# Optimization experiments

Measured on AMD Instinct MI355X. Metric: run time of the kernel, lower is better.

The kernel has to match this reference:

```python
import jax, jax.numpy as jnp
from jax import lax
import numpy as np

B, T, H, L = 4096, 7, 512, 256
D = 2 * H  # bidirectional LSTM feature dim


def _lstm(x, wih, whh, bih, bhh, reverse):
    # x: [B, T, L]; torch gate order i, f, g, o
    b, hdim = x.shape[0], whh.shape[0]
    xs = jnp.swapaxes(x, 0, 1)  # [T, B, L]
    bias = bih + bhh

    def step(carry, xt):
        h, c = carry
        gates = xt @ wih + h @ whh + bias
        i, f, g, o = jnp.split(gates, 4, axis=-1)
        c = jax.nn.sigmoid(f) * c + jax.nn.sigmoid(i) * jnp.tanh(g)
        h = jax.nn.sigmoid(o) * jnp.tanh(c)
        return (h, c), h

    h0 = jnp.zeros((b, hdim), x.dtype)
    _, hs = lax.scan(step, (h0, h0), xs, reverse=reverse)
    return jnp.swapaxes(hs, 0, 1)  # [B, T, H]


def _att(enc, dec):
    # Sequential attention: keys/values start as enc and grow with each decoder output.
    keys = enc  # [B, T, D]
    outs = []
    for i in range(dec.shape[1]):  # fixed small T=7, Python loop is static
        q = dec[:, i, :]                                  # [B, D]
        scores = jnp.einsum('bd,btd->bt', q, keys)        # dot over features
        a = jax.nn.softmax(scores, axis=1)
        ctx = jnp.einsum('bt,btd->bd', a, keys)
        out = ctx + q
        outs.append(out)
        keys = jnp.concatenate([keys, out[:, None, :]], axis=1)
    return jnp.stack(outs, axis=1)  # [B, T, D]


def _deconv(x, w, b):
    # torch ConvTranspose2d (stride 1, pad 0) == full conv with flipped, in/out-swapped kernel
    kh, kw = w.shape[2], w.shape[3]
    w2 = jnp.transpose(w[:, :, ::-1, ::-1], (1, 0, 2, 3))  # [out, in, kh, kw]
    y = lax.conv_general_dilated(x, w2, (1, 1), ((kh - 1, kh - 1), (kw - 1, kw - 1)),
                                 dimension_numbers=('NCHW', 'OIHW', 'NCHW'))
    return y + b[None, :, None, None]


def setup_inputs() -> dict:
    key = jax.random.key(0)
    ks = jax.random.split(key, 12)
    p = lambda k, shape: jax.random.normal(k, shape, jnp.float32) * 0.02
    return {
        'lstm_enc': jax.random.normal(ks[0], (B, T, D), jnp.float32),
        'gaussian_noise': jax.random.normal(ks[1], (B, L), jnp.float32),
        'embedrep_w': p(ks[2], (L, L * T)), 'embedrep_b': jnp.zeros((L * T,), jnp.float32),
        'wih_f': p(ks[3], (L, 4 * H)), 'whh_f': p(ks[4], (H, 4 * H)),
        'bih_f': jnp.zeros((4 * H,), jnp.float32), 'bhh_f': jnp.zeros((4 * H,), jnp.float32),
        'wih_b': p(ks[5], (L, 4 * H)), 'whh_b': p(ks[6], (H, 4 * H)),
        'bih_b': jnp.zeros((4 * H,), jnp.float32), 'bhh_b': jnp.zeros((4 * H,), jnp.float32),
        'emb_w': p(ks[7], (D, 1024)), 'emb_b': jnp.zeros((1024,), jnp.float32),
        'dc3_w': p(ks[8], (64, 32, 1, 3)), 'dc3_b': jnp.zeros((32,), jnp.float32),
        'dc1_w': p(ks[9], (32, 16, 1, 5)), 'dc1_b': jnp.zeros((16,), jnp.float32),
        'dc2_w': p(ks[10], (16, 1, 3, 3)), 'dc2_b': jnp.zeros((1,), jnp.float32),
        'infer': 0,
    }


def reference(lstm_enc, gaussian_noise, embedrep_w, embedrep_b,
              wih_f, whh_f, bih_f, bhh_f, wih_b, whh_b, bih_b, bhh_b,
              emb_w, emb_b, dc3_w, dc3_b, dc1_w, dc1_b, dc2_w, dc2_b, infer):
    b = lstm_enc.shape[0]
    g1 = jax.nn.soft_sign(gaussian_noise @ embedrep_w + embedrep_b)   # [B, L*T]
    rep = g1.reshape(b, T, L)                                          # [B, 7, L]
    hf = _lstm(rep, wih_f, whh_f, bih_f, bhh_f, False)
    hb = _lstm(rep, wih_b, whh_b, bih_b, bhh_b, True)
    lstm1 = jnp.concatenate([hf, hb], axis=-1)                         # [B, 7, 2H]
    att_out = _att(lstm_enc, lstm1)                                    # [B, 7, 2H]
    emb = att_out @ emb_w + emb_b                                      # [B, 7, 1024]
    up = jax.nn.soft_sign(emb).reshape(b * T, 64, 1, 16)
    x = jax.nn.leaky_relu(_deconv(up, dc3_w, dc3_b))                   # [B*7, 32, 1, 18]
    x = jax.nn.leaky_relu(_deconv(x, dc1_w, dc1_b))                    # [B*7, 16, 1, 22]
    x = jax.nn.leaky_relu(_deconv(x, dc2_w, dc2_b))                    # [B*7, 1, 3, 24]
    x = jax.nn.softmax(x, axis=2)                                      # softmax over H dim (=3)
    out = x.reshape(b, T, 1, 3, 24)[:, :, -1, :, :]                    # [B, 7, 3, 24]
    return out
```

## Files before the change

### kernel.cpp

```cpp
#include <hip/hip_runtime.h>
#include <stdint.h>


typedef __attribute__((ext_vector_type(4))) float f32x4;
typedef __attribute__((ext_vector_type(8))) short bf16x8;
typedef __attribute__((ext_vector_type(4))) unsigned short us4;

__device__ __forceinline__ unsigned short f2b(float f) {
  union { float f; unsigned u; } x; x.f = f;
  unsigned r = x.u + 0x7FFFu + ((x.u >> 16) & 1u);
  return (unsigned short)(r >> 16);
}
__device__ __forceinline__ float b2f(unsigned short s) {
  union { unsigned u; float f; } x; x.u = ((unsigned)s) << 16; return x.f;
}
__device__ __forceinline__ float sigmoidf(float x) {
  return 1.f / (1.f + __expf(-x));
}
__device__ __forceinline__ float fast_tanh(float x) {
  x = fminf(15.f, fmaxf(-15.f, x));
  float e = __expf(2.f * x);
  return (e - 1.f) / (e + 1.f);
}

__device__ __forceinline__ void gl_lds16(const void* g, void* l) {
  auto gp = reinterpret_cast<const __attribute__((address_space(1))) unsigned int*>(
      reinterpret_cast<uintptr_t>(g));
  auto lp = reinterpret_cast<__attribute__((address_space(3))) unsigned int*>(
      reinterpret_cast<uintptr_t>(l));
  __builtin_amdgcn_global_load_lds(gp, lp, 16, 0, 0);
}


__device__ __forceinline__ void stage256x32(const unsigned short* src, int ld,
                                            unsigned short* hbase, int tid) {
  const int row_in = tid >> 2;
  const int gidx = tid & 3;
#pragma unroll
  for (int r = 0; r < 4; ++r) {
    int row = r * 64 + row_in;
    int gsrc = gidx ^ ((row >> 1) & 3);
    gl_lds16(src + (size_t)row * ld + gsrc * 8, hbase + r * 2048 + (tid >> 6) * 512);
  }
}

__device__ __forceinline__ void stage128x32(const unsigned short* src, int ld,
                                            unsigned short* hbase, int tid) {
  const int row_in = tid >> 2;
  const int gidx = tid & 3;
#pragma unroll
  for (int r = 0; r < 2; ++r) {
    int row = r * 64 + row_in;
    int gsrc = gidx ^ ((row >> 1) & 3);
    gl_lds16(src + (size_t)row * ld + gsrc * 8, hbase + r * 2048 + (tid >> 6) * 512);
  }
}

__device__ __forceinline__ bf16x8 lds_fragH(const unsigned short* hbase, int row, int lq) {
  return *(const bf16x8*)(hbase + row * 32 + (lq ^ (((row >> 1) & 3) << 3)));
}

__device__ __forceinline__ void tile_w128(const unsigned short* Ab, const unsigned short* Bb,
                                          int wm, int wn, int lane, f32x4 (&acc)[8][4]) {
  const int lr = lane & 15, lq = (lane >> 4) * 8;
  bf16x8 b[4];
#pragma unroll
  for (int n = 0; n < 4; ++n) b[n] = lds_fragH(Bb, wn * 64 + n * 16 + lr, lq);
  bf16x8 a[8];
#pragma unroll
  for (int i = 0; i < 8; ++i) a[i] = lds_fragH(Ab, wm * 128 + i * 16 + lr, lq);
  __builtin_amdgcn_s_setprio(1);
#pragma unroll
  for (int i = 0; i < 8; ++i)
#pragma unroll
    for (int n = 0; n < 4; ++n)
      acc[i][n] = __builtin_amdgcn_mfma_f32_16x16x32_bf16(a[i], b[n], acc[i][n], 0, 0, 0);
  __builtin_amdgcn_s_setprio(0);
}

#define DBUF_SYNC()                                   \
  asm volatile("s_waitcnt vmcnt(0)" ::: "memory");    \
  __builtin_amdgcn_s_barrier();                       \
  __builtin_amdgcn_sched_barrier(0);

__device__ __forceinline__ void stage128x64(const unsigned short* src, int ld,
                                            unsigned short* lds, int wv, int lane) {
#pragma unroll
  for (int r = 0; r < 4; ++r) {
    int row = r * 32 + wv * 8 + (lane >> 3);
    gl_lds16(src + (size_t)row * ld + (lane & 7) * 8, lds + (r * 32 + wv * 8) * 64);
  }
}
__device__ __forceinline__ void mfma_tile(const unsigned short* As, const unsigned short* Bs,
                                          int wm, int wn, int lane, f32x4 acc[4][4]) {
#pragma unroll
  for (int kk = 0; kk < 2; ++kk) {
    int ko = kk * 32 + (lane >> 4) * 8;
    bf16x8 a[4], b[4];
#pragma unroll
    for (int i = 0; i < 4; ++i)
      a[i] = *(const bf16x8*)(As + (size_t)(wm * 64 + i * 16 + (lane & 15)) * 64 + ko);
#pragma unroll
    for (int i = 0; i < 4; ++i)
      b[i] = *(const bf16x8*)(Bs + (size_t)(wn * 64 + i * 16 + (lane & 15)) * 64 + ko);
#pragma unroll
    for (int mi = 0; mi < 4; ++mi)
#pragma unroll
      for (int ni = 0; ni < 4; ++ni)
        acc[mi][ni] = __builtin_amdgcn_mfma_f32_16x16x32_bf16(a[mi], b[ni], acc[mi][ni], 0, 0, 0);
  }
}

__global__ __launch_bounds__(256) void pack_kernel(
    const float* __restrict__ noise, const float* __restrict__ erep_w,
    const float* __restrict__ emb_w,
    const float* __restrict__ wih_f, const float* __restrict__ whh_f,
    const float* __restrict__ bih_f, const float* __restrict__ bhh_f,
    const float* __restrict__ wih_b, const float* __restrict__ whh_b,
    const float* __restrict__ bih_b, const float* __restrict__ bhh_b,
    unsigned short* __restrict__ noiseb, unsigned short* __restrict__ erepT,
    unsigned short* __restrict__ embT, unsigned short* __restrict__ lstmW,
    float* __restrict__ lstmB) {
  const int N0 = 4096 * 256 / 4;
  const int N1 = 1792 * 256 / 4;
  const int N2 = 1024 * 1024 / 4;
  const int N3 = 2 * 2048 * 768 / 4;
  const int N4 = 2 * 2048 / 4;
  const int total = N0 + N1 + N2 + N3 + N4;
  for (int i = blockIdx.x * 256 + threadIdx.x; i < total; i += gridDim.x * 256) {
    int x = i;
    if (x < N0) {
      f32x4 v = ((const f32x4*)noise)[x];
      us4 o4;
#pragma unroll
      for (int e = 0; e < 4; ++e) o4[e] = f2b(v[e]);
      ((us4*)noiseb)[x] = o4;
      continue;
    }
    x -= N0;
    if (x < N1) {
      int n = x >> 6, k4 = (x & 63) * 4;
      us4 o4;
#pragma unroll
      for (int e = 0; e < 4; ++e) o4[e] = f2b(erep_w[(size_t)(k4 + e) * 1792 + n]);
      ((us4*)erepT)[x] = o4;
      continue;
    }
    x -= N1;
    if (x < N2) {
      int n = x >> 8, k4 = (x & 255) * 4;
      int o = (n & 63) * 16 + (n >> 6);
      us4 o4;
#pragma unroll
      for (int e = 0; e < 4; ++e) o4[e] = f2b(emb_w[(size_t)(k4 + e) * 1024 + o]);
      ((us4*)embT)[x] = o4;
      continue;
    }
    x -= N2;
    if (x < N3) {
      int dir = x / (2048 * 192);
      int r = x - dir * (2048 * 192);
      int npk = r / 192, k4 = (r - npk * 192) * 4;
      int blk = npk >> 6, g = (npk >> 4) & 3, u = npk & 15;
      int o = g * 512 + blk * 16 + u;
      const float* wih = dir ? wih_b : wih_f;
      const float* whh = dir ? whh_b : whh_f;
      us4 o4;
#pragma unroll
      for (int e = 0; e < 4; ++e) {
        int k = k4 + e;
        float v = (k < 256) ? wih[(size_t)k * 2048 + o] : whh[(size_t)(k - 256) * 2048 + o];
        o4[e] = f2b(v);
      }
      ((us4*)lstmW)[x] = o4;
      continue;
    }
    x -= N3;
    {
      int dir = x >> 9, npk4 = (x & 511) * 4;
      int blk = npk4 >> 6, g = (npk4 >> 4) & 3, u = npk4 & 15;
      int o = g * 512 + blk * 16 + u;
      const float* bi = dir ? bih_b : bih_f;
      const float* bh = dir ? bhh_b : bhh_f;
      f32x4 o4;
#pragma unroll
      for (int e = 0; e < 4; ++e) o4[e] = bi[o + e] + bh[o + e];
      ((f32x4*)lstmB)[x] = o4;
    }
  }
}

__global__ __launch_bounds__(256) void gemm_rep_kernel(
    const unsigned short* __restrict__ A, const unsigned short* __restrict__ Bt,
    const float* __restrict__ bias, unsigned short* __restrict__ rep_t) {
  __shared__ unsigned short As[128 * 64];
  __shared__ unsigned short Bs[128 * 64];
  const int lane = threadIdx.x & 63, wv = threadIdx.x >> 6;
  const int wm = wv >> 1, wn = wv & 1;
  const int m0 = blockIdx.y * 128, n0 = blockIdx.x * 128;
  f32x4 acc[4][4];
#pragma unroll
  for (int i = 0; i < 4; ++i)
#pragma unroll
    for (int j = 0; j < 4; ++j) acc[i][j] = (f32x4){0.f, 0.f, 0.f, 0.f};
  for (int k0 = 0; k0 < 256; k0 += 64) {
    stage128x64(A + (size_t)m0 * 256 + k0, 256, As, wv, lane);
    stage128x64(Bt + (size_t)n0 * 256 + k0, 256, Bs, wv, lane);
    __syncthreads();
    mfma_tile(As, Bs, wm, wn, lane, acc);
    __syncthreads();
  }
#pragma unroll
  for (int ni = 0; ni < 4; ++ni) {
    int n = n0 + wn * 64 + ni * 16 + (lane & 15);
    float bv = bias[n];
    int t = n >> 8, l = n & 255;
#pragma unroll
    for (int mi = 0; mi < 4; ++mi)
#pragma unroll
      for (int r = 0; r < 4; ++r) {
        int m = m0 + wm * 64 + mi * 16 + (lane >> 4) * 4 + r;
        float v = acc[mi][ni][r] + bv;
        v = v / (1.f + fabsf(v));
        rep_t[((size_t)t * 4096 + m) * 256 + l] = f2b(v);
      }
  }
}

template <int NT>
__global__ __launch_bounds__(256, 2) void lstm_step_kernel(
    const unsigned short* __restrict__ rep_t, const unsigned short* __restrict__ Wp,
    const float* __restrict__ biasP, unsigned short* __restrict__ cbuf,
    unsigned short* __restrict__ lstm1, int step) {
  __shared__ unsigned short Ar[2][8192];
  __shared__ unsigned short Br[2][4096];
  const int tid = threadIdx.x, lane = tid & 63, wv = tid >> 6;
  const int wm = wv >> 1, wn = wv & 1;
  const int swz = (blockIdx.x & 7) * 64 + (blockIdx.x >> 3);
  const int dir = swz >> 8;
  const int rem = swz & 255;
  const int by = rem >> 4, bx = rem & 15;
  const int m0 = by * 256, n0 = bx * 128;
  const int t_proc = dir ? (6 - step) : step;
  const int t_prev = dir ? (t_proc + 1) : (t_proc - 1);
  const unsigned short* W = Wp + (size_t)dir * 2048 * 768;
  unsigned short* cp = cbuf + (size_t)dir * (4096 * 512);
  const unsigned short* xsrc = rep_t + (size_t)t_proc * 4096 * 256;
  const unsigned short* hsrc =
      lstm1 + (size_t)((NT == 24) ? t_prev : 0) * 1024 + (size_t)dir * 512;

  f32x4 acc[8][4];
#pragma unroll
  for (int i = 0; i < 8; ++i)
#pragma unroll
    for (int j = 0; j < 4; ++j) acc[i][j] = (f32x4){0.f, 0.f, 0.f, 0.f};

  auto asrc = [&](int tt) {
    return tt < 8 ? xsrc + (size_t)m0 * 256 + tt * 32
                  : hsrc + (size_t)m0 * 7168 + (tt - 8) * 32;
  };
  auto ald = [&](int tt) { return tt < 8 ? 256 : 7168; };

  stage256x32(asrc(0), ald(0), Ar[0], tid);
  stage128x32(W + (size_t)n0 * 768 + 0 * 32, 768, Br[0], tid);
  DBUF_SYNC()

#pragma unroll
  for (int t = 0; t < NT; ++t) {
    if (t + 1 < NT) {
      stage256x32(asrc(t + 1), ald(t + 1), Ar[(t + 1) & 1], tid);
      stage128x32(W + (size_t)n0 * 768 + (t + 1) * 32, 768, Br[(t + 1) & 1], tid);
    }
    tile_w128(Ar[t & 1], Br[t & 1], wm, wn, lane, acc);
    if (t + 1 < NT) { DBUF_SYNC() }
  }

  const int u = lane & 15;
  const int blk = (n0 + wn * 64) >> 6;
  const int j = blk * 16 + u;
  const float bz0 = biasP[dir * 2048 + blk * 64 + 0 * 16 + u];
  const float bz1 = biasP[dir * 2048 + blk * 64 + 1 * 16 + u];
  const float bz2 = biasP[dir * 2048 + blk * 64 + 2 * 16 + u];
  const float bz3 = biasP[dir * 2048 + blk * 64 + 3 * 16 + u];
#pragma unroll
  for (int mi = 0; mi < 8; ++mi)
#pragma unroll
    for (int r = 0; r < 4; ++r) {
      int row = m0 + wm * 128 + mi * 16 + (lane >> 4) * 4 + r;
      float gi = acc[mi][0][r] + bz0;
      float gf = acc[mi][1][r] + bz1;
      float gg = acc[mi][2][r] + bz2;
      float go = acc[mi][3][r] + bz3;
      size_t ci = (size_t)row * 512 + j;
      float c;
      if (NT == 8) {
        c = sigmoidf(gi) * fast_tanh(gg);
      } else {
        c = sigmoidf(gf) * b2f(cp[ci]) + sigmoidf(gi) * fast_tanh(gg);
      }
      cp[ci] = f2b(c);
      float h = sigmoidf(go) * fast_tanh(c);
      lstm1[((size_t)row * 7 + t_proc) * 1024 + dir * 512 + j] = f2b(h);
    }
}

__global__ __launch_bounds__(256) void att_fused3_kernel(
    const float* __restrict__ enc, const unsigned short* __restrict__ lstm1,
    unsigned short* __restrict__ att) {
  __shared__ unsigned short Qs[7 * 1032];
  __shared__ unsigned short Es[7 * 1032];
  __shared__ float P[8 * 256];
  __shared__ float sG[98];
  __shared__ float sC[7][14];
  __shared__ float sA[16];
  const int tid = threadIdx.x, lane = tid & 63, wv = tid >> 6;
  const int b = blockIdx.x;
  const float* Eb = enc + (size_t)b * 7168;
  const unsigned short* Qb = lstm1 + (size_t)b * 7168;

  if (tid < 98) ((float*)sC)[tid] = 0.f;

  const f32x4* Eb4 = (const f32x4*)Eb;
  const int d0 = tid * 4;
#pragma unroll
  for (int r = 0; r < 7; ++r) {
    f32x4 v = Eb4[r * 256 + tid];
    us4 hi;
#pragma unroll
    for (int e = 0; e < 4; ++e) hi[e] = f2b(v[e]);
    *(us4*)&Es[r * 1032 + d0] = hi;
    *(us4*)&Qs[r * 1032 + d0] = *(const us4*)(Qb + r * 1024 + d0);
  }
  asm volatile("s_waitcnt lgkmcnt(0)" ::: "memory");
  __builtin_amdgcn_sched_barrier(0);

  {
    const int rr = lane & 15;
    const int rowc = rr % 7;
    const int kbase = wv * 256 + (lane >> 4) * 8;
    f32x4 g1 = {0.f, 0.f, 0.f, 0.f}, g2 = {0.f, 0.f, 0.f, 0.f};
#pragma unroll
    for (int s = 0; s < 8; ++s) {
      const int k0 = kbase + s * 32;
      bf16x8 aq = *(const bf16x8*)&Qs[rowc * 1032 + k0];
      bf16x8 be = *(const bf16x8*)&Es[rowc * 1032 + k0];
      g1 = __builtin_amdgcn_mfma_f32_16x16x32_bf16(aq, be, g1, 0, 0, 0);
      g2 = __builtin_amdgcn_mfma_f32_16x16x32_bf16(aq, aq, g2, 0, 0, 0);
    }
    *(f32x4*)&P[((wv * 2 + 0) * 64 + lane) * 4] = g1;
    *(f32x4*)&P[((wv * 2 + 1) * 64 + lane) * 4] = g2;
  }
  __syncthreads();

  if (tid < 98) {
    int i = tid / 14, v = tid - i * 14;
    int col = v < 7 ? v : v - 7;
    int tile = v < 7 ? 0 : 1;
    int ln = ((i >> 2) << 4) | col;
    int rg = i & 3;
    float s = 0.f;
#pragma unroll
    for (int w = 0; w < 4; ++w) s += P[((w * 2 + tile) * 64 + ln) * 4 + rg];
    sG[i * 14 + v] = s;
  }
  __syncthreads();
  if (wv == 0) {
    for (int i = 0; i < 7; ++i) {
      const int nt = 7 + i;
      float s = -1e30f;
      if (lane < 7) {
        s = sG[i * 14 + lane];
      } else if (lane < nt) {
        int jj = lane - 7;
        float a2 = 0.f;
#pragma unroll
        for (int v = 0; v < 14; ++v) a2 += sC[jj][v] * sG[i * 14 + v];
        s = a2;
      }
      float mx = s;
#pragma unroll
      for (int off = 8; off >= 1; off >>= 1) mx = fmaxf(mx, __shfl_xor(mx, off, 16));
      float e = (lane < nt) ? __expf(s - mx) : 0.f;
      float sum = e;
#pragma unroll
      for (int off = 8; off >= 1; off >>= 1) sum += __shfl_xor(sum, off, 16);
      float aw = e / sum;
      if (lane < 16) sA[lane] = aw;
      if (lane < 14) {
        float c = (lane < 7) ? sA[lane] : 0.f;
        for (int jj = 0; jj < i; ++jj) c += sA[7 + jj] * sC[jj][lane];
        if (lane == 7 + i) c += 1.f;
        sC[i][lane] = c;
      }
    }
  }
  __syncthreads();

  {
    float acc[7][4];
#pragma unroll
    for (int i = 0; i < 7; ++i)
#pragma unroll
      for (int e = 0; e < 4; ++e) acc[i][e] = 0.f;
#pragma unroll
    for (int t = 0; t < 7; ++t) {
      us4 ev = *(const us4*)&Es[t * 1032 + d0];
      float evf[4];
#pragma unroll
      for (int e = 0; e < 4; ++e) evf[e] = b2f(ev[e]);
#pragma unroll
      for (int i = 0; i < 7; ++i) {
        float c = sC[i][t];
#pragma unroll
        for (int e = 0; e < 4; ++e) acc[i][e] += c * evf[e];
      }
    }
#pragma unroll
    for (int m = 0; m < 7; ++m) {
      us4 qv = *(const us4*)&Qs[m * 1032 + d0];
      float qf[4];
#pragma unroll
      for (int e = 0; e < 4; ++e) qf[e] = b2f(qv[e]);
#pragma unroll
      for (int i = m; i < 7; ++i) {
        float c = sC[i][7 + m];
#pragma unroll
        for (int e = 0; e < 4; ++e) acc[i][e] += c * qf[e];
      }
    }
    unsigned short* Ab = att + (size_t)b * 7168;
#pragma unroll
    for (int i = 0; i < 7; ++i) {
      us4 r;
#pragma unroll
      for (int e = 0; e < 4; ++e) r[e] = f2b(acc[i][e]);
      *(us4*)(Ab + i * 1024 + d0) = r;
    }
  }
}

__global__ __launch_bounds__(256, 2) void gemm_emb_kernel(
    const unsigned short* __restrict__ A, const unsigned short* __restrict__ Bt,
    const float* __restrict__ bias, unsigned short* __restrict__ up_t) {
  __shared__ unsigned short Ar[2][8192];
  __shared__ unsigned short Br[2][4096];
  const int tid = threadIdx.x, lane = tid & 63, wv = tid >> 6;
  const int wm = wv >> 1, wn = wv & 1;
  const int swz = (blockIdx.x & 7) * 112 + (blockIdx.x >> 3);
  const int by = swz >> 3, bx = swz & 7;
  const int m0 = by * 256, n0 = bx * 128;

  f32x4 acc[8][4];
#pragma unroll
  for (int i = 0; i < 8; ++i)
#pragma unroll
    for (int j = 0; j < 4; ++j) acc[i][j] = (f32x4){0.f, 0.f, 0.f, 0.f};

  const unsigned short* Abase = A + (size_t)m0 * 1024;
  const unsigned short* Bbase = Bt + (size_t)n0 * 1024;

  stage256x32(Abase + 0 * 32, 1024, Ar[0], tid);
  stage128x32(Bbase + 0 * 32, 1024, Br[0], tid);
  DBUF_SYNC()

#pragma unroll
  for (int t = 0; t < 32; ++t) {
    if (t + 1 < 32) {
      stage256x32(Abase + (t + 1) * 32, 1024, Ar[(t + 1) & 1], tid);
      stage128x32(Bbase + (t + 1) * 32, 1024, Br[(t + 1) & 1], tid);
    }
    tile_w128(Ar[t & 1], Br[t & 1], wm, wn, lane, acc);
    if (t + 1 < 32) { DBUF_SYNC() }
  }

#pragma unroll
  for (int ni = 0; ni < 4; ++ni) {
    int np = n0 + wn * 64 + ni * 16 + (lane & 15);
    int o = (np & 63) * 16 + (np >> 6);
    float bv = bias[o];
#pragma unroll
    for (int mi = 0; mi < 8; ++mi)
#pragma unroll
      for (int r = 0; r < 4; ++r) {
        int m = m0 + wm * 128 + mi * 16 + (lane >> 4) * 4 + r;
        float v = acc[mi][ni][r] + bv;
        v = v / (1.f + fabsf(v));
        up_t[(size_t)m * 1024 + np] = f2b(v);
      }
  }
}

__global__ __launch_bounds__(256) void dc_fused_kernel(
    const unsigned short* __restrict__ up_t,
    const float* __restrict__ w3, const float* __restrict__ b3,
    const float* __restrict__ w1, const float* __restrict__ b1,
    const float* __restrict__ w2, const float* __restrict__ b2,
    float* __restrict__ out) {
  __shared__ unsigned short y1L[576 * 40];
  __shared__ unsigned short y2L[704 * 24];
  const int tid = threadIdx.x, lane = tid & 63, wv = tid >> 6;
  const int g0 = blockIdx.x * 32;
  const int kq = (lane >> 4) * 8;
  const int oc = lane & 15;

  {
    bf16x8 bf[2][6];
#pragma unroll
    for (int nt = 0; nt < 2; ++nt)
#pragma unroll
      for (int kk = 0; kk < 6; ++kk) {
        bf16x8 v;
#pragma unroll
        for (int t = 0; t < 8; ++t) {
          int k = kk * 32 + kq + t;
          int jj = k >> 6, ic = k & 63;
          v[t] = (short)f2b(w3[((size_t)ic * 32 + nt * 16 + oc) * 3 + jj]);
        }
        bf[nt][kk] = v;
      }
    const float bia0 = b3[oc], bia1 = b3[16 + oc];
    for (int c = wv; c < 36; c += 4) {
      int m = c * 16 + (lane & 15);
      int imgl = m / 18, ow = m - imgl * 18;
      const unsigned short* arow = up_t + (size_t)(g0 + imgl) * 1024;
      f32x4 acc0 = {0.f, 0.f, 0.f, 0.f}, acc1 = {0.f, 0.f, 0.f, 0.f};
#pragma unroll
      for (int kk = 0; kk < 6; ++kk) {
        int jj = kk >> 1;
        int ic0 = (kk & 1) * 32 + kq;
        int iw = ow - jj;
        bf16x8 a = {0, 0, 0, 0, 0, 0, 0, 0};
        if ((unsigned)iw < 16u) a = *(const bf16x8*)(arow + iw * 64 + ic0);
        acc0 = __builtin_amdgcn_mfma_f32_16x16x32_bf16(a, bf[0][kk], acc0, 0, 0, 0);
        acc1 = __builtin_amdgcn_mfma_f32_16x16x32_bf16(a, bf[1][kk], acc1, 0, 0, 0);
      }
#pragma unroll
      for (int r = 0; r < 4; ++r) {
        int mm = c * 16 + (lane >> 4) * 4 + r;
        float v0 = acc0[r] + bia0; v0 = v0 > 0.f ? v0 : 0.01f * v0;
        float v1 = acc1[r] + bia1; v1 = v1 > 0.f ? v1 : 0.01f * v1;
        y1L[mm * 40 + oc] = f2b(v0);
        y1L[mm * 40 + 16 + oc] = f2b(v1);
      }
    }
  }
  __syncthreads();

  {
    bf16x8 bf[5];
#pragma unroll
    for (int kk = 0; kk < 5; ++kk) {
      bf16x8 v;
#pragma unroll
      for (int t = 0; t < 8; ++t) {
        int ic = kq + t;
        v[t] = (short)f2b(w1[((size_t)ic * 16 + oc) * 5 + kk]);
      }
      bf[kk] = v;
    }
    const float bia = b1[oc];
    for (int c = wv; c < 44; c += 4) {
      int m = c * 16 + (lane & 15);
      int imgl = m / 22, ow = m - imgl * 22;
      const unsigned short* abase = y1L + imgl * (18 * 40);
      f32x4 acc = {0.f, 0.f, 0.f, 0.f};
#pragma unroll
      for (int kk = 0; kk < 5; ++kk) {
        int iw = ow - kk;
        bf16x8 a = {0, 0, 0, 0, 0, 0, 0, 0};
        if ((unsigned)iw < 18u) a = *(const bf16x8*)(abase + iw * 40 + kq);
        acc = __builtin_amdgcn_mfma_f32_16x16x32_bf16(a, bf[kk], acc, 0, 0, 0);
      }
#pragma unroll
      for (int r = 0; r < 4; ++r) {
        int mm = c * 16 + (lane >> 4) * 4 + r;
        float v = acc[r] + bia;
        v = v > 0.f ? v : 0.01f * v;
        y2L[mm * 24 + oc] = f2b(v);
      }
    }
  }
  __syncthreads();

  for (int ii = tid; ii < 768; ii += 256) {
    int imgl = ii / 24, ow = ii - imgl * 24;
    float lg0 = b2[0], lg1 = b2[0], lg2 = b2[0];
#pragma unroll
    for (int jj = 0; jj < 3; ++jj) {
      int iw = ow - jj;
      if ((unsigned)iw >= 22u) continue;
      const unsigned short* row = y2L + (imgl * 22 + iw) * 24;
      bf16x8 v0 = *(const bf16x8*)(row);
      bf16x8 v1 = *(const bf16x8*)(row + 8);
      float x[16];
#pragma unroll
      for (int ic = 0; ic < 8; ++ic) {
        x[ic] = b2f((unsigned short)v0[ic]);
        x[8 + ic] = b2f((unsigned short)v1[ic]);
      }
#pragma unroll
      for (int ic = 0; ic < 16; ++ic) {
        lg0 += x[ic] * w2[ic * 9 + 0 * 3 + jj];
        lg1 += x[ic] * w2[ic * 9 + 1 * 3 + jj];
        lg2 += x[ic] * w2[ic * 9 + 2 * 3 + jj];
      }
    }
    lg0 = lg0 > 0.f ? lg0 : 0.01f * lg0;
    lg1 = lg1 > 0.f ? lg1 : 0.01f * lg1;
    lg2 = lg2 > 0.f ? lg2 : 0.01f * lg2;
    float mx = fmaxf(lg0, fmaxf(lg1, lg2));
    float e0 = __expf(lg0 - mx), e1 = __expf(lg1 - mx), e2 = __expf(lg2 - mx);
    float inv = 1.f / (e0 + e1 + e2);
    size_t ob = (size_t)(g0 + imgl) * 72 + ow;
    out[ob] = e0 * inv;
    out[ob + 24] = e1 * inv;
    out[ob + 48] = e2 * inv;
  }
}

extern "C" void kernel_launch(void* const* d_in, const int* in_sizes, int n_in,
                              void* d_out, int out_size, void* d_ws, size_t ws_size,
                              hipStream_t stream) {
  (void)in_sizes; (void)n_in; (void)out_size; (void)ws_size;
  const float* enc    = (const float*)d_in[0];
  const float* noise  = (const float*)d_in[1];
  const float* erep_w = (const float*)d_in[2];
  const float* erep_b = (const float*)d_in[3];
  const float* wih_f  = (const float*)d_in[4];
  const float* whh_f  = (const float*)d_in[5];
  const float* bih_f  = (const float*)d_in[6];
  const float* bhh_f  = (const float*)d_in[7];
  const float* wih_b  = (const float*)d_in[8];
  const float* whh_b  = (const float*)d_in[9];
  const float* bih_b  = (const float*)d_in[10];
  const float* bhh_b  = (const float*)d_in[11];
  const float* emb_w  = (const float*)d_in[12];
  const float* emb_b  = (const float*)d_in[13];
  const float* dc3w   = (const float*)d_in[14];
  const float* dc3b   = (const float*)d_in[15];
  const float* dc1w   = (const float*)d_in[16];
  const float* dc1b   = (const float*)d_in[17];
  const float* dc2w   = (const float*)d_in[18];
  const float* dc2b   = (const float*)d_in[19];
  float* out = (float*)d_out;

  char* p = (char*)d_ws;
  auto carve = [&p](size_t bytes) {
    char* r = p;
    p += (bytes + 255) & ~(size_t)255;
    return r;
  };
  unsigned short* rep_t  = (unsigned short*)carve(7ull * 4096 * 256 * 2);
  unsigned short* lstmW  = (unsigned short*)carve(2ull * 2048 * 768 * 2);
  float*          lstmB  = (float*)carve(2ull * 2048 * 4);
  unsigned short* noiseb = (unsigned short*)carve(4096ull * 256 * 2);
  unsigned short* erepT  = (unsigned short*)carve(1792ull * 256 * 2);
  unsigned short* embT   = (unsigned short*)carve(1024ull * 1024 * 2);
  unsigned short* cbuf   = (unsigned short*)carve(2ull * 4096 * 512 * 2);
  unsigned short* lstm1  = (unsigned short*)carve(4096ull * 7 * 1024 * 2);
  unsigned short* att    = (unsigned short*)carve(28672ull * 1024 * 2);
  unsigned short* up_t   = (unsigned short*)carve(28672ull * 1024 * 2);

  pack_kernel<<<2048, 256, 0, stream>>>(noise, erep_w, emb_w, wih_f, whh_f, bih_f, bhh_f,
                                        wih_b, whh_b, bih_b, bhh_b,
                                        noiseb, erepT, embT, lstmW, lstmB);
  gemm_rep_kernel<<<dim3(14, 32), 256, 0, stream>>>(noiseb, erepT, erep_b, rep_t);
  lstm_step_kernel<8><<<512, 256, 0, stream>>>(rep_t, lstmW, lstmB, cbuf, lstm1, 0);
  for (int s = 1; s < 7; ++s)
    lstm_step_kernel<24><<<512, 256, 0, stream>>>(rep_t, lstmW, lstmB, cbuf, lstm1, s);
  att_fused3_kernel<<<4096, 256, 0, stream>>>(enc, lstm1, att);
  gemm_emb_kernel<<<896, 256, 0, stream>>>(att, embT, emb_b, up_t);
  dc_fused_kernel<<<896, 256, 0, stream>>>(up_t, dc3w, dc3b, dc1w, dc1b, dc2w, dc2b, out);
}
```

Baseline: 468.7 us.

## Rewrite embedding GEMM as 512-thread 256x256 tile with 4-stage ping-pong pipeline

```diff
diff --git a/kernel.cpp b/kernel.cpp
--- a/kernel.cpp
+++ b/kernel.cpp
@@ -31,6 +31,13 @@
   __builtin_amdgcn_global_load_lds(gp, lp, 16, 0, 0);
 }
 
+template <int N>
+__device__ __forceinline__ void gate() {
+  if constexpr (N == 8) asm volatile("s_waitcnt vmcnt(8)" ::: "memory");
+  else if constexpr (N == 4) asm volatile("s_waitcnt vmcnt(4)" ::: "memory");
+  else asm volatile("s_waitcnt vmcnt(0)" ::: "memory");
+}
+
 
 __device__ __forceinline__ void stage256x32(const unsigned short* src, int ld,
                                             unsigned short* hbase, int tid) {
@@ -53,6 +60,18 @@
     int row = r * 64 + row_in;
     int gsrc = gidx ^ ((row >> 1) & 3);
     gl_lds16(src + (size_t)row * ld + gsrc * 8, hbase + r * 2048 + (tid >> 6) * 512);
+  }
+}
+
+__device__ __forceinline__ void stage256x32_t512(const unsigned short* src, int ld,
+                                                 unsigned short* hbase, int tid) {
+  const int row_in = tid >> 2;
+  const int gidx = tid & 3;
+#pragma unroll
+  for (int r = 0; r < 2; ++r) {
+    int row = r * 128 + row_in;
+    int gsrc = gidx ^ ((row >> 1) & 3);
+    gl_lds16(src + (size_t)row * ld + gsrc * 8, hbase + r * 4096 + (tid >> 6) * 512);
   }
 }
 
@@ -439,16 +458,16 @@
   }
 }
 
-__global__ __launch_bounds__(256, 2) void gemm_emb_kernel(
+__global__ __launch_bounds__(512, 1) void gemm_emb8p_kernel(
     const unsigned short* __restrict__ A, const unsigned short* __restrict__ Bt,
     const float* __restrict__ bias, unsigned short* __restrict__ up_t) {
-  __shared__ unsigned short Ar[2][8192];
-  __shared__ unsigned short Br[2][4096];
+  __shared__ unsigned short Ar[4][8192];
+  __shared__ unsigned short Br[4][8192];
   const int tid = threadIdx.x, lane = tid & 63, wv = tid >> 6;
-  const int wm = wv >> 1, wn = wv & 1;
-  const int swz = (blockIdx.x & 7) * 112 + (blockIdx.x >> 3);
-  const int by = swz >> 3, bx = swz & 7;
-  const int m0 = by * 256, n0 = bx * 128;
+  const int wm = wv >> 2, wn = wv & 3;
+  const int swz = (blockIdx.x & 7) * 56 + (blockIdx.x >> 3);
+  const int by = swz >> 2, bx = swz & 3;
+  const int m0 = by * 256, n0 = bx * 256;
 
   f32x4 acc[8][4];
 #pragma unroll
@@ -458,19 +477,57 @@
 
   const unsigned short* Abase = A + (size_t)m0 * 1024;
   const unsigned short* Bbase = Bt + (size_t)n0 * 1024;
-
-  stage256x32(Abase + 0 * 32, 1024, Ar[0], tid);
-  stage128x32(Bbase + 0 * 32, 1024, Br[0], tid);
-  DBUF_SYNC()
-
-#pragma unroll
+  const int lr = lane & 15, lq = (lane >> 4) * 8;
+
+  stage256x32_t512(Abase + 0 * 32, 1024, Ar[0], tid);
+  stage256x32_t512(Bbase + 0 * 32, 1024, Br[0], tid);
+  stage256x32_t512(Abase + 1 * 32, 1024, Ar[1], tid);
+  stage256x32_t512(Bbase + 1 * 32, 1024, Br[1], tid);
+  stage256x32_t512(Abase + 2 * 32, 1024, Ar[2], tid);
+  stage256x32_t512(Bbase + 2 * 32, 1024, Br[2], tid);
+  gate<8>();
+  __builtin_amdgcn_s_barrier();
+  __builtin_amdgcn_sched_barrier(0);
+
   for (int t = 0; t < 32; ++t) {
+    const unsigned short* Ab = Ar[t & 3];
+    const unsigned short* Bb = Br[t & 3];
+    bf16x8 b[4], a0[4], a1[4];
+#pragma unroll
+    for (int n = 0; n < 4; ++n) b[n] = lds_fragH(Bb, wn * 64 + n * 16 + lr, lq);
+#pragma unroll
+    for (int i = 0; i < 4; ++i) a0[i] = lds_fragH(Ab, wm * 128 + i * 16 + lr, lq);
+    if (t + 3 < 32) stage256x32_t512(Abase + (t + 3) * 32, 1024, Ar[(t + 3) & 3], tid);
+    __builtin_amdgcn_sched_barrier(0);
+    __builtin_amdgcn_s_barrier();
+    asm volatile("s_waitcnt lgkmcnt(0)" ::: "memory");
+    __builtin_amdgcn_sched_barrier(0);
+    __builtin_amdgcn_s_setprio(1);
+#pragma unroll
+    for (int i = 0; i < 4; ++i)
+#pragma unroll
+      for (int n = 0; n < 4; ++n)
+        acc[i][n] = __builtin_amdgcn_mfma_f32_16x16x32_bf16(a0[i], b[n], acc[i][n], 0, 0, 0);
+    __builtin_amdgcn_s_setprio(0);
+#pragma unroll
+    for (int i = 0; i < 4; ++i) a1[i] = lds_fragH(Ab, wm * 128 + (4 + i) * 16 + lr, lq);
+    if (t + 3 < 32) stage256x32_t512(Bbase + (t + 3) * 32, 1024, Br[(t + 3) & 3], tid);
     if (t + 1 < 32) {
-      stage256x32(Abase + (t + 1) * 32, 1024, Ar[(t + 1) & 1], tid);
-      stage128x32(Bbase + (t + 1) * 32, 1024, Br[(t + 1) & 1], tid);
-    }
-    tile_w128(Ar[t & 1], Br[t & 1], wm, wn, lane, acc);
-    if (t + 1 < 32) { DBUF_SYNC() }
+      if (t <= 28) gate<8>();
+      else if (t == 29) gate<4>();
+      else gate<0>();
+    }
+    __builtin_amdgcn_sched_barrier(0);
+    __builtin_amdgcn_s_barrier();
+    asm volatile("s_waitcnt lgkmcnt(0)" ::: "memory");
+    __builtin_amdgcn_sched_barrier(0);
+    __builtin_amdgcn_s_setprio(1);
+#pragma unroll
+    for (int i = 0; i < 4; ++i)
+#pragma unroll
+      for (int n = 0; n < 4; ++n)
+        acc[4 + i][n] = __builtin_amdgcn_mfma_f32_16x16x32_bf16(a1[i], b[n], acc[4 + i][n], 0, 0, 0);
+    __builtin_amdgcn_s_setprio(0);
   }
 
 #pragma unroll
@@ -669,6 +726,6 @@
   for (int s = 1; s < 7; ++s)
     lstm_step_kernel<24><<<512, 256, 0, stream>>>(rep_t, lstmW, lstmB, cbuf, lstm1, s);
   att_fused3_kernel<<<4096, 256, 0, stream>>>(enc, lstm1, att);
-  gemm_emb_kernel<<<896, 256, 0, stream>>>(att, embT, emb_b, up_t);
+  gemm_emb8p_kernel<<<448, 512, 0, stream>>>(att, embT, emb_b, up_t);
   dc_fused_kernel<<<896, 256, 0, stream>>>(up_t, dc3w, dc3b, dc1w, dc1b, dc2w, dc2b, out);
 }
```

New measurement: 469.6 us. About the same (+0.2%).
